# Optimization experiments

Hardware: AMD Instinct MI355X
Metric: run time of the kernel (lower is better)

The kernel has to match this reference:

```python
import jax, jax.numpy as jnp
import numpy as np

N_NODES = 32768
N_GRAPHS = 16
N_PER = N_NODES // N_GRAPHS  # 2048 nodes per graph
N_EDGES = 262144
D = 128      # node_state_dim
DE = 64      # edge_state_dim
H = 256      # edge hidden / message dim (= 2*D, required by matching prop)
NH = 256     # node MLP hidden


def _mlp2(x, W1, b1, W2, b2):
    # Linear -> ReLU -> Linear (torch nn.Linear convention: y = x @ W.T + b)
    return jax.nn.relu(x @ W1.T + b1) @ W2.T + b2


def setup_inputs() -> dict:
    key = jax.random.key(0)
    ks = jax.random.split(key, 16)
    s = 0.1  # edge_net_init_scale-ish small init
    inp = {
        "node_states": jax.random.normal(ks[0], (N_NODES, D), jnp.float32),
        "edge_features": jax.random.normal(ks[1], (N_EDGES, DE), jnp.float32),
        "from_idx": jax.random.randint(ks[2], (N_EDGES,), 0, N_NODES, jnp.int32),
        "to_idx": jax.random.randint(ks[3], (N_EDGES,), 0, N_NODES, jnp.int32),
        "graph_idx": jnp.repeat(jnp.arange(N_GRAPHS, dtype=jnp.int32), N_PER),
        "n_graphs": N_GRAPHS,
        # forward message net: Linear(2D+DE -> H), Linear(H -> H)
        "Wm1": jax.random.normal(ks[4], (H, 2 * D + DE), jnp.float32) * s,
        "bm1": jnp.zeros((H,), jnp.float32),
        "Wm2": jax.random.normal(ks[5], (H, H), jnp.float32) * s,
        "bm2": jnp.zeros((H,), jnp.float32),
        # reverse message net (separate params)
        "Wr1": jax.random.normal(ks[6], (H, 2 * D + DE), jnp.float32) * s,
        "br1": jnp.zeros((H,), jnp.float32),
        "Wr2": jax.random.normal(ks[7], (H, H), jnp.float32) * s,
        "br2": jnp.zeros((H,), jnp.float32),
        # node update MLP: Linear(4D -> NH), Linear(NH -> D)
        "Wn1": jax.random.normal(ks[8], (NH, 4 * D), jnp.float32) * s,
        "bn1": jnp.zeros((NH,), jnp.float32),
        "Wn2": jax.random.normal(ks[9], (D, NH), jnp.float32) * s,
        "bn2": jnp.zeros((D,), jnp.float32),
    }
    return inp


def _forward(node_states, edge_features, from_idx, to_idx, n_graphs,
             Wm1, bm1, Wm2, bm2, Wr1, br1, Wr2, br2, Wn1, bn1, Wn2, bn2):
    n = node_states.shape[0]
    fs = node_states[from_idx]   # [E, D] gather
    ts = node_states[to_idx]     # [E, D]
    # forward direction: messages -> scatter-add into to_idx
    m_fwd = _mlp2(jnp.concatenate([fs, ts, edge_features], -1), Wm1, bm1, Wm2, bm2)
    agg = jax.ops.segment_sum(m_fwd, to_idx, num_segments=n)
    # reverse direction: swap endpoints, scatter-add into from_idx
    m_rev = _mlp2(jnp.concatenate([ts, fs, edge_features], -1), Wr1, br1, Wr2, br2)
    agg = agg + jax.ops.segment_sum(m_rev, from_idx, num_segments=n)

    # cross-graph dual-softmax attention over (i, i+1) graph pairs.
    # graph_idx is contiguous equal-size blocks -> reshape partitioning.
    n_per = n // n_graphs
    d = node_states.reshape(n_graphs // 2, 2, n_per, -1)
    x, y = d[:, 0], d[:, 1]                      # [P, Np, D] each
    a = jnp.einsum('pid,pjd->pij', x, y)         # dotproduct similarity
    a_x = jax.nn.softmax(a, axis=2)              # softmax over y per x-row
    a_y = jax.nn.softmax(a, axis=1)              # softmax over x per y-col
    attn_x = jnp.einsum('pij,pjd->pid', a_x, y)  # [P, Np, D]
    attn_y = jnp.einsum('pij,pid->pjd', a_y, x)  # [P, Np, D]
    cross = jnp.stack([attn_x, attn_y], axis=1).reshape(n, -1)

    attention_input = node_states - cross
    node_inputs = jnp.concatenate([agg, attention_input, node_states], -1)  # [N, 4D]
    mlp_out = _mlp2(node_inputs, Wn1, bn1, Wn2, bn2)
    return node_states + mlp_out  # residual update


def reference(node_states, edge_features, from_idx, to_idx, graph_idx, n_graphs,
              Wm1, bm1, Wm2, bm2, Wr1, br1, Wr2, br2, Wn1, bn1, Wn2, bn2):
    return _forward(node_states, edge_features, from_idx, to_idx, int(n_graphs),
                    Wm1, bm1, Wm2, bm2, Wr1, br1, Wr2, br2, Wn1, bn1, Wn2, bn2)
```

## Files before the change

kernel.cpp:

```cpp
#include <hip/hip_runtime.h>


typedef __bf16 bf16_t;
typedef __bf16 bf16x8 __attribute__((ext_vector_type(8)));
typedef __bf16 bf16x4 __attribute__((ext_vector_type(4)));
typedef float  f32x4  __attribute__((ext_vector_type(4)));

#define MFMA16(a,b,c) __builtin_amdgcn_mfma_f32_16x16x32_bf16((a),(b),(c),0,0,0)

constexpr int NNODES = 32768;
constexpr int NEDGES = 262144;
constexpr int DD = 128;
constexpr int HH = 256;

__device__ __forceinline__ bf16x8 cvt8(f32x4 a, f32x4 b){
  bf16x8 r;
  r[0]=(bf16_t)a[0]; r[1]=(bf16_t)a[1]; r[2]=(bf16_t)a[2]; r[3]=(bf16_t)a[3];
  r[4]=(bf16_t)b[0]; r[5]=(bf16_t)b[1]; r[6]=(bf16_t)b[2]; r[7]=(bf16_t)b[3];
  return r;
}

__global__ void cvt_kernel(const float* __restrict__ in, bf16_t* __restrict__ out, int n){
  int i = (blockIdx.x*256 + threadIdx.x)*4;
  if (i < n){
    f32x4 v = *(const f32x4*)(in + i);
    bf16x4 o; o[0]=(bf16_t)v[0]; o[1]=(bf16_t)v[1]; o[2]=(bf16_t)v[2]; o[3]=(bf16_t)v[3];
    *(bf16x4*)(out + i) = o;
  }
}

__global__ void cvt_wp_kernel(const float* __restrict__ Wm1, const float* __restrict__ Wr1,
                              bf16_t* __restrict__ wp){
  int idx = (blockIdx.x*256 + threadIdx.x)*4;
  int n = idx >> 7, k = idx & 127;
  const float* W = (n < 512) ? Wm1 : Wr1;
  int row = n & 255;
  int colbase = ((n >> 8) & 1) * 128;
  f32x4 v = *(const f32x4*)(W + (size_t)row*320 + colbase + k);
  bf16x4 o; o[0]=(bf16_t)v[0]; o[1]=(bf16_t)v[1]; o[2]=(bf16_t)v[2]; o[3]=(bf16_t)v[3];
  *(bf16x4*)(wp + idx) = o;
}

__global__ void pack_wc_kernel(const float* __restrict__ Wm1, const float* __restrict__ Wr1,
                               bf16_t* __restrict__ wc){
  int g = blockIdx.x*256 + threadIdx.x;
  int part = g >> 11, gg = g & 2047;
  int tile = gg >> 6, lane = gg & 63;
  int kc = tile >> 4, nt = tile & 15;
  int lr = lane & 15, lk = lane >> 4;
  const float* W = part ? Wr1 : Wm1;
  int row = nt*16 + lr;
  int col = 256 + kc*32 + lk*8;
  f32x4 v0 = *(const f32x4*)(W + (size_t)row*320 + col);
  f32x4 v1 = *(const f32x4*)(W + (size_t)row*320 + col + 4);
  *(bf16x8*)(wc + (size_t)g*8) = cvt8(v0,v1);
}

__global__ void pack_wn2_kernel(const float* __restrict__ Wn2, bf16_t* __restrict__ out){
  int g = blockIdx.x*256 + threadIdx.x;
  int tile = g >> 6, lane = g & 63;
  int kc = tile >> 3, nt = tile & 7;
  int lr = lane & 15, lk = lane >> 4;
  int row = nt*16 + lr;
  int col = kc*32 + lk*8;
  f32x4 v0 = *(const f32x4*)(Wn2 + (size_t)row*256 + col);
  f32x4 v1 = *(const f32x4*)(Wn2 + (size_t)row*256 + col + 4);
  *(bf16x8*)(out + (size_t)g*8) = cvt8(v0,v1);
}

__global__ void hist_kernel(const int* __restrict__ to_idx, const int* __restrict__ from_idx,
                            int* __restrict__ cnt_to, int* __restrict__ cnt_from){
  int e = blockIdx.x*256 + threadIdx.x;
  if (e < NEDGES){
    atomicAdd(&cnt_to[to_idx[e]], 1);
    atomicAdd(&cnt_from[from_idx[e]], 1);
  }
}

__global__ void scan_kernel(int* __restrict__ cnt, int* __restrict__ start){
  __shared__ int sums[1024];
  const int t = threadIdx.x;
  int local[32]; int s = 0;
  #pragma unroll
  for (int j=0;j<32;j++){ local[j] = cnt[t*32+j]; s += local[j]; }
  sums[t] = s; __syncthreads();
  #pragma unroll
  for (int d=1; d<1024; d<<=1){
    int v = (t>=d) ? sums[t-d] : 0;
    __syncthreads();
    sums[t] += v;
    __syncthreads();
  }
  int off = sums[t] - s;
  #pragma unroll
  for (int j=0;j<32;j++){
    start[t*32+j] = off;
    cnt[t*32+j]   = off;
    off += local[j];
  }
  if (t == 1023) start[32768] = sums[1023];
}

__global__ void place_kernel(const int* __restrict__ to_idx, const int* __restrict__ from_idx,
                             int* __restrict__ cur_to, int* __restrict__ cur_from,
                             int* __restrict__ eid_to, int* __restrict__ eid_from,
                             int* __restrict__ rowv_to, int* __restrict__ rowv_from){
  int e = blockIdx.x*256 + threadIdx.x;
  if (e < NEDGES){
    int vt = to_idx[e];
    int p = atomicAdd(&cur_to[vt], 1);
    eid_to[p] = e;
    rowv_to[p] = vt;
    int vf = from_idx[e];
    int q = atomicAdd(&cur_from[vf], 1);
    eid_from[q] = e;
    rowv_from[q] = vf;
  }
}

__global__ __launch_bounds__(256,3) void proj_kernel(
    const float* __restrict__ ns, const bf16_t* __restrict__ Wp,
    bf16_t* __restrict__ P1, bf16_t* __restrict__ P2)
{
  constexpr int XS = 136;
  constexpr int CS = 264;
  __shared__ bf16_t Xs[64*XS];
  __shared__ bf16_t Cs[64*CS];
  const int tid = threadIdx.x;
  const int rb = blockIdx.x*64;
  const int cb = blockIdx.y;
  #pragma unroll
  for (int it=0; it<8; ++it){
    int c = tid + it*256;
    int row = c >> 5, co = (c & 31)*4;
    f32x4 v = *(const f32x4*)(ns + (size_t)(rb+row)*DD + co);
    bf16x4 o; o[0]=(bf16_t)v[0]; o[1]=(bf16_t)v[1]; o[2]=(bf16_t)v[2]; o[3]=(bf16_t)v[3];
    *(bf16x4*)&Xs[row*XS + co] = o;
  }
  __syncthreads();
  const int lane = tid & 63, wave = tid >> 6, lr = lane & 15, lk = lane >> 4;
  const bf16_t* Wb = Wp + (size_t)cb*256*128;
  f32x4 acc[16];
  #pragma unroll
  for (int nt=0;nt<16;nt++) acc[nt] = (f32x4){0.f,0.f,0.f,0.f};
  #pragma unroll
  for (int kc=0;kc<4;kc++){
    bf16x8 a = *(const bf16x8*)&Xs[(wave*16 + lr)*XS + kc*32 + lk*8];
    #pragma unroll
    for (int nt=0;nt<16;nt++){
      bf16x8 b = *(const bf16x8*)&Wb[(size_t)(nt*16 + lr)*128 + kc*32 + lk*8];
      acc[nt] = MFMA16(a,b,acc[nt]);
    }
  }
  #pragma unroll
  for (int nt=0;nt<16;nt++)
    #pragma unroll
    for (int r=0;r<4;r++)
      Cs[(wave*16 + lk*4 + r)*CS + nt*16 + lr] = (bf16_t)acc[nt][r];
  __syncthreads();
  bf16_t* P = cb ? P2 : P1;
  #pragma unroll
  for (int it=0; it<8; ++it){
    int c = tid + it*256;
    int row = c >> 5, co = (c & 31)*8;
    *(bf16x8*)&P[(size_t)(rb+row)*HH + co] = *(const bf16x8*)&Cs[row*CS + co];
  }
}

__global__ __launch_bounds__(256,4) void edge_agg_kernel(
    const float* __restrict__ ef, const bf16_t* __restrict__ Wc,
    const int* __restrict__ eid, const int* __restrict__ oth,
    const int* __restrict__ rowv, const int* __restrict__ start,
    const bf16_t* __restrict__ P1, const bf16_t* __restrict__ P2,
    const float* __restrict__ b1,
    float* __restrict__ partial, bf16_t* __restrict__ aggh)
{
  constexpr int CS = 264;
  __shared__ bf16_t Cs[64*CS];
  __shared__ int es[64], os[64], vs[64];
  const int tid = threadIdx.x;
  const int rb = blockIdx.x*64;
  if (tid < 64){
    int e = eid[rb + tid];
    es[tid] = e;
    os[tid] = oth[e];
    vs[tid] = rowv[rb + tid];
  }
  __syncthreads();

  const int lane = tid & 63, wave = tid >> 6, lr = lane & 15, lk = lane >> 4;
  {
    const float* arow = ef + (size_t)es[wave*16 + lr]*64;
    bf16x8 a0, a1;
    {
      f32x4 v0 = *(const f32x4*)(arow + lk*8);
      f32x4 v1 = *(const f32x4*)(arow + lk*8 + 4);
      a0 = cvt8(v0,v1);
      f32x4 w0 = *(const f32x4*)(arow + 32 + lk*8);
      f32x4 w1 = *(const f32x4*)(arow + 32 + lk*8 + 4);
      a1 = cvt8(w0,w1);
    }
    #pragma unroll
    for (int p=0;p<2;p++){
      f32x4 acc[8];
      #pragma unroll
      for (int nt=0;nt<8;nt++) acc[nt] = (f32x4){0.f,0.f,0.f,0.f};
      #pragma unroll
      for (int nt=0;nt<8;nt++){
        bf16x8 b0 = *(const bf16x8*)&Wc[(size_t)((0*16 + p*8 + nt)*64 + lane)*8];
        acc[nt] = MFMA16(a0,b0,acc[nt]);
        bf16x8 b1v = *(const bf16x8*)&Wc[(size_t)((1*16 + p*8 + nt)*64 + lane)*8];
        acc[nt] = MFMA16(a1,b1v,acc[nt]);
      }
      #pragma unroll
      for (int nt=0;nt<8;nt++)
        #pragma unroll
        for (int r=0;r<4;r++)
          Cs[(wave*16 + lk*4 + r)*CS + (p*8+nt)*16 + lr] = (bf16_t)acc[nt][r];
    }
  }
  __syncthreads();

  const int c8 = (tid & 31) * 8;
  const int rbase = (tid >> 5) * 8;
  {
    f32x4 b1a = *(const f32x4*)(b1 + c8);
    f32x4 b1b = *(const f32x4*)(b1 + c8 + 4);
    #pragma unroll
    for (int j=0;j<8;j++){
      const int row = rbase + j;
      bf16x8 cs = *(const bf16x8*)&Cs[row*CS + c8];
      bf16x8 p1 = *(const bf16x8*)&P1[(size_t)os[row]*HH + c8];
      bf16x8 p2 = *(const bf16x8*)&P2[(size_t)vs[row]*HH + c8];
      bf16x8 o;
      #pragma unroll
      for (int k=0;k<4;k++){
        o[k]   = (bf16_t)fmaxf((float)cs[k]   + (float)p1[k]   + (float)p2[k]   + b1a[k], 0.f);
        o[4+k] = (bf16_t)fmaxf((float)cs[4+k] + (float)p1[4+k] + (float)p2[4+k] + b1b[k], 0.f);
      }
      *(bf16x8*)&Cs[row*CS + c8] = o;
    }
  }
  __syncthreads();

  const int c = tid;
  float runsum = 0.f;
  int curv = vs[0];
  for (int row=0; row<64; ++row){
    const int v = vs[row];
    if (v != curv){
      const int s0 = start[curv], s1 = start[curv+1];
      if (s0 >= rb && s1 <= rb+64)
        aggh[(size_t)curv*HH + c] = (bf16_t)runsum;
      else
        partial[((size_t)curv*2 + (s0 >= rb ? 0 : 1))*HH + c] = runsum;
      runsum = 0.f; curv = v;
    }
    runsum += (float)Cs[row*CS + c];
  }
  {
    const int s0 = start[curv], s1 = start[curv+1];
    if (s0 >= rb && s1 <= rb+64)
      aggh[(size_t)curv*HH + c] = (bf16_t)runsum;
    else
      partial[((size_t)curv*2 + (s0 >= rb ? 0 : 1))*HH + c] = runsum;
  }
}

__global__ __launch_bounds__(256) void combine_kernel(
    const float* __restrict__ partial, const int* __restrict__ start,
    bf16_t* __restrict__ aggh)
{
  const int tid = threadIdx.x;
  const int v = blockIdx.x*8 + (tid>>5);
  const int c0 = (tid & 31)*8;
  const int s0 = start[v], s1 = start[v+1];
  if (s1 == s0){
    bf16x8 z;
    #pragma unroll
    for (int j=0;j<8;j++) z[j] = (bf16_t)0.f;
    *(bf16x8*)&aggh[(size_t)v*HH + c0] = z;
  } else if ((s0>>6) != ((s1-1)>>6)){
    const float* p0 = partial + ((size_t)v*2    )*HH + c0;
    const float* p1 = partial + ((size_t)v*2 + 1)*HH + c0;
    f32x4 a0 = *(const f32x4*)p0;
    f32x4 a1 = *(const f32x4*)(p0+4);
    f32x4 c1 = *(const f32x4*)p1;
    f32x4 c2 = *(const f32x4*)(p1+4);
    bf16x8 o;
    #pragma unroll
    for (int j=0;j<4;j++){ o[j]=(bf16_t)(a0[j]+c1[j]); o[4+j]=(bf16_t)(a1[j]+c2[j]); }
    *(bf16x8*)&aggh[(size_t)v*HH + c0] = o;
  }
}

__global__ __launch_bounds__(256) void w2t_kernel(const float* __restrict__ Wm2, const float* __restrict__ Wr2,
                                                  bf16_t* __restrict__ wm2T, bf16_t* __restrict__ wr2T){
  __shared__ bf16_t t[64][72];
  const int bi = (blockIdx.x & 3)*64;
  const int bj = ((blockIdx.x>>2) & 3)*64;
  const int m  = blockIdx.x >> 4;
  const float* W = m ? Wr2 : Wm2;
  bf16_t* WT = m ? wr2T : wm2T;
  const int tid = threadIdx.x;
  #pragma unroll
  for (int it=0; it<16; ++it){
    int c = tid + it*256;
    int r = c >> 6, co = c & 63;
    t[r][co] = (bf16_t)W[(size_t)(bi+r)*256 + bj + co];
  }
  __syncthreads();
  #pragma unroll
  for (int it=0; it<16; ++it){
    int c = tid + it*256;
    int r = c >> 6, co = c & 63;
    WT[(size_t)(bj+r)*256 + bi + co] = t[co][r];
  }
}

__global__ __launch_bounds__(256,2) void wcat_gemm_kernel(
    const float* __restrict__ Wn1, const bf16_t* __restrict__ wm2T, const bf16_t* __restrict__ wr2T,
    bf16_t* __restrict__ wcat)
{
  constexpr int XS = 264, CS = 264;
  __shared__ bf16_t Xs[64*XS];
  __shared__ bf16_t Cs[64*CS];
  const int tid = threadIdx.x;
  const int rb = blockIdx.x*64;
  const int cb = blockIdx.y;
  const bf16_t* BT = cb ? wr2T : wm2T;
  #pragma unroll
  for (int it=0; it<16; ++it){
    int c = tid + it*256;
    int row = c >> 6, co = (c & 63)*4;
    f32x4 v = *(const f32x4*)(Wn1 + (size_t)(rb+row)*512 + co);
    bf16x4 o; o[0]=(bf16_t)v[0]; o[1]=(bf16_t)v[1]; o[2]=(bf16_t)v[2]; o[3]=(bf16_t)v[3];
    *(bf16x4*)&Xs[row*XS + co] = o;
  }
  __syncthreads();
  const int lane = tid & 63, wave = tid >> 6, lr = lane & 15, lk = lane >> 4;
  f32x4 acc[16];
  #pragma unroll
  for (int nt=0;nt<16;nt++) acc[nt] = (f32x4){0.f,0.f,0.f,0.f};
  #pragma unroll
  for (int kc=0;kc<8;kc++){
    bf16x8 a = *(const bf16x8*)&Xs[(wave*16 + lr)*XS + kc*32 + lk*8];
    #pragma unroll
    for (int nt=0;nt<16;nt++){
      bf16x8 b = *(const bf16x8*)&BT[(size_t)(nt*16 + lr)*256 + kc*32 + lk*8];
      acc[nt] = MFMA16(a,b,acc[nt]);
    }
  }
  #pragma unroll
  for (int nt=0;nt<16;nt++)
    #pragma unroll
    for (int r=0;r<4;r++)
      Cs[(wave*16 + lk*4 + r)*CS + nt*16 + lr] = (bf16_t)acc[nt][r];
  __syncthreads();
  const int nt_base = rb >> 4;
  #pragma unroll
  for (int it=0; it<8; ++it){
    int g = tid + it*256;
    int tile = g >> 6, lane2 = g & 63;
    int kc_l = tile >> 2, nt_l = tile & 3;
    int lr2 = lane2 & 15, lk2 = lane2 >> 4;
    bf16x8 v = *(const bf16x8*)&Cs[(nt_l*16 + lr2)*CS + kc_l*32 + lk2*8];
    *(bf16x8*)&wcat[(size_t)(((cb*8 + kc_l)*16 + nt_base + nt_l)*64 + lane2)*8] = v;
  }
}

__global__ void wcat_copy_kernel(const float* __restrict__ Wn1, bf16_t* __restrict__ wcat){
  int g = blockIdx.x*256 + threadIdx.x;
  int tile = g >> 6, lane = g & 63;
  int kc = tile >> 4, nt = tile & 15;
  int lr = lane & 15, lk = lane >> 4;
  int row = nt*16 + lr;
  int col = 256 + kc*32 + lk*8;
  f32x4 v0 = *(const f32x4*)(Wn1 + (size_t)row*512 + col);
  f32x4 v1 = *(const f32x4*)(Wn1 + (size_t)row*512 + col + 4);
  *(bf16x8*)&wcat[(size_t)(((16 + kc)*16 + nt)*64 + lane)*8] = cvt8(v0,v1);
}

__global__ __launch_bounds__(256) void uw_kernel(const float* __restrict__ Wn1,
    const float* __restrict__ bm2, const float* __restrict__ br2,
    float* __restrict__ u, float* __restrict__ w){
  const int n = threadIdx.x;
  float su=0.f, sw=0.f;
  for (int j=0;j<256;j+=4){
    f32x4 wv = *(const f32x4*)(Wn1 + (size_t)n*512 + j);
    f32x4 bu = *(const f32x4*)(bm2 + j);
    f32x4 bw = *(const f32x4*)(br2 + j);
    #pragma unroll
    for (int q=0;q<4;q++){ su += wv[q]*bu[q]; sw += wv[q]*bw[q]; }
  }
  u[n]=su; w[n]=sw;
}

__global__ __launch_bounds__(256) void nst_kernel(const float* __restrict__ ns, bf16_t* __restrict__ nsT){
  constexpr int XS2 = 136;
  __shared__ bf16_t Xs[64*XS2];
  const int tid = threadIdx.x;
  const int nb = blockIdx.x*64;
  #pragma unroll
  for (int it=0; it<8; ++it){
    int c = tid + it*256;
    int rowl = c >> 5, co = (c & 31)*4;
    f32x4 v = *(const f32x4*)(ns + (size_t)(nb+rowl)*DD + co);
    bf16x4 o; o[0]=(bf16_t)v[0]; o[1]=(bf16_t)v[1]; o[2]=(bf16_t)v[2]; o[3]=(bf16_t)v[3];
    *(bf16x4*)&Xs[rowl*XS2 + co] = o;
  }
  __syncthreads();
  const int sb = nb >> 11;
  const int jb = nb & 2047;
  bf16_t* outp = nsT + (size_t)sb*DD*2048 + jb;
  #pragma unroll
  for (int it=0; it<4; ++it){
    int c = tid + it*256;
    int d = c >> 3, g8 = (c & 7)*8;
    bf16x8 o;
    #pragma unroll
    for (int k=0;k<8;k++){
      int s64 = g8 + k;
      int t32 = s64 >> 5, s = s64 & 31;
      int m = (s & 1) ? (16 + (s>>1)) : (s>>1);
      o[k] = Xs[(t32*32 + m)*XS2 + d];
    }
    *(bf16x8*)(outp + (size_t)d*2048 + g8) = o;
  }
}

__global__ __launch_bounds__(256,2) void attn_kernel(
    const bf16_t* __restrict__ nsB, const bf16_t* __restrict__ nsT,
    const float* __restrict__ ns, bf16_t* __restrict__ attnB)
{
  constexpr int KS = 136;
  constexpr int VS = 40;
  constexpr int PS = 40;
  __shared__ bf16_t Ks[2][32*KS];
  __shared__ bf16_t Vt[2][128*VS];
  __shared__ bf16_t Ps[64*PS];
  const int tid = threadIdx.x;
  const int lane = tid & 63, wave = tid >> 6, lr = lane & 15, lk = lane >> 4;
  const int bx = blockIdx.x;
  const int qt = bx & 31, side = (bx>>5)&1, p = bx>>6;
  const size_t qbase = (size_t)p*4096 + (size_t)side*2048 + (size_t)qt*64;
  const int sbkv = p*2 + (side^1);
  const bf16_t* Kv = nsB + ((size_t)p*4096 + (size_t)(side^1)*2048)*DD;
  const bf16_t* Vp = nsT + (size_t)sbkv*DD*2048;

  bf16x8 qf[4];
  {
    const bf16_t* qrow = nsB + (qbase + wave*16 + lr)*DD;
    #pragma unroll
    for (int kc=0;kc<4;kc++) qf[kc] = *(const bf16x8*)(qrow + kc*32 + lk*8);
  }
  float ls[4] = {0.f,0.f,0.f,0.f};
  f32x4 acco[8];
  #pragma unroll
  for (int nt=0;nt<8;nt++) acco[nt]=(f32x4){0.f,0.f,0.f,0.f};

  const int krow0 = tid>>4,        kcol = (tid&15)*8;
  const int vd0   = tid>>2,        vsl  = (tid&3)*8;
  bf16x8 kreg0, kreg1, vreg0, vreg1;

  auto load_tile = [&](int t){
    const bf16_t* kp = Kv + (size_t)t*32*DD;
    kreg0 = *(const bf16x8*)(kp + (size_t)krow0*DD + kcol);
    kreg1 = *(const bf16x8*)(kp + (size_t)(krow0+16)*DD + kcol);
    const bf16_t* vp = Vp + t*32;
    vreg0 = *(const bf16x8*)(vp + (size_t)vd0*2048 + vsl);
    vreg1 = *(const bf16x8*)(vp + (size_t)(vd0+64)*2048 + vsl);
  };
  auto store_tile = [&](int b){
    *(bf16x8*)&Ks[b][krow0*KS + kcol]      = kreg0;
    *(bf16x8*)&Ks[b][(krow0+16)*KS + kcol] = kreg1;
    *(bf16x8*)&Vt[b][vd0*VS + vsl]         = vreg0;
    *(bf16x8*)&Vt[b][(vd0+64)*VS + vsl]    = vreg1;
  };

  load_tile(0);
  store_tile(0);
  load_tile(1);
  __syncthreads();
  int cur = 0;
  for (int t=0; t<64; ++t){
    if (t+1 < 64){
      store_tile(cur^1);
      if (t+2 < 64) load_tile(t+2);
    }
    f32x4 s0 = (f32x4){0.f,0.f,0.f,0.f}, s1 = (f32x4){0.f,0.f,0.f,0.f};
    #pragma unroll
    for (int kc=0;kc<4;kc++){
      bf16x8 b0 = *(const bf16x8*)&Ks[cur][lr*KS      + kc*32 + lk*8];
      bf16x8 b1 = *(const bf16x8*)&Ks[cur][(16+lr)*KS + kc*32 + lk*8];
      s0 = MFMA16(qf[kc], b0, s0);
      s1 = MFMA16(qf[kc], b1, s1);
    }
    #pragma unroll
    for (int r=0;r<4;r++){
      float p0 = __expf(s0[r] - 40.f);
      float p1 = __expf(s1[r] - 40.f);
      ls[r] += p0 + p1;
      union { bf16_t h[2]; unsigned u; } pk;
      pk.h[0] = (bf16_t)p0; pk.h[1] = (bf16_t)p1;
      *(unsigned*)&Ps[(wave*16 + lk*4 + r)*PS + 2*lr] = pk.u;
    }
    asm volatile("s_waitcnt lgkmcnt(0)" ::: "memory");
    __builtin_amdgcn_sched_barrier(0);
    bf16x8 pa = *(const bf16x8*)&Ps[(wave*16 + lr)*PS + lk*8];
    #pragma unroll
    for (int nt=0;nt<8;nt++){
      bf16x8 vb = *(const bf16x8*)&Vt[cur][(nt*16+lr)*VS + lk*8];
      acco[nt] = MFMA16(pa, vb, acco[nt]);
    }
    __syncthreads();
    cur ^= 1;
  }
  #pragma unroll
  for (int r=0;r<4;r++){
    float v = ls[r];
    v += __shfl_xor(v,1); v += __shfl_xor(v,2);
    v += __shfl_xor(v,4); v += __shfl_xor(v,8);
    ls[r] = 1.f/v;
  }
  #pragma unroll
  for (int nt=0;nt<8;nt++){
    const int col = nt*16 + lr;
    #pragma unroll
    for (int r=0;r<4;r++){
      const size_t row = qbase + wave*16 + lk*4 + r;
      attnB[row*DD + col] = (bf16_t)(ns[row*DD + col] - acco[nt][r]*ls[r]);
    }
  }
}

__global__ __launch_bounds__(256,2) void node_mlp_kernel(
    const bf16_t* __restrict__ agghf, const bf16_t* __restrict__ agghr,
    const bf16_t* __restrict__ attnB, const bf16_t* __restrict__ nsB,
    const float* __restrict__ ns,
    const bf16_t* __restrict__ wcat, const float* __restrict__ bn1,
    const float* __restrict__ uvec, const float* __restrict__ wvec,
    const int* __restrict__ start_to, const int* __restrict__ start_from,
    const bf16_t* __restrict__ Wn2b, const float* __restrict__ bn2,
    float* __restrict__ out)
{
  __shared__ __align__(16) bf16_t As[32*768];
  bf16_t* Hs = As;
  const int tid = threadIdx.x;
  const int lane = tid & 63, wave = tid >> 6, lr = lane & 15, lk = lane >> 4;
  const int rb = blockIdx.x*32;

  bf16x8 stg[12];
  int dsta[12];
  #pragma unroll
  for (int it=0; it<12; ++it){
    const int db = it*4096 + tid*16;
    const int row = db / 1536;
    const int within = db - row*1536;
    const size_t node = (size_t)(rb + row);
    const char* s0 = (const char*)agghf + (node<<9) + within;
    const char* s1 = (const char*)agghr + (node<<9) + (within-512);
    const char* s2 = (const char*)attnB + (node<<8) + (within-1024);
    const char* s3 = (const char*)nsB   + (node<<8) + (within-1280);
    const char* src = within < 512 ? s0 : (within < 1024 ? s1 : (within < 1280 ? s2 : s3));
    stg[it] = *(const bf16x8*)src;
    dsta[it] = row*1536 + (within ^ ((row & 7) << 4));
  }
  #pragma unroll
  for (int it=0; it<12; ++it)
    *(bf16x8*)((char*)As + dsta[it]) = stg[it];
  __syncthreads();

  const int cg = wave >> 1;
  const int colbase = cg * 128;
  const int arow = (wave & 1)*16 + lr;
  const unsigned abase = (unsigned)arow * 1536u;
  const unsigned asw = ((unsigned)(arow & 7)) << 4;
  f32x4 acc[8];
  #pragma unroll
  for (int nt=0;nt<8;nt++) acc[nt] = (f32x4){0.f,0.f,0.f,0.f};
  #pragma unroll
  for (int kc=0; kc<24; ++kc){
    const unsigned y = (unsigned)(kc*64 + lk*16);
    bf16x8 a = *(const bf16x8*)((const char*)As + abase + (y ^ asw));
    #pragma unroll
    for (int nt=0;nt<8;nt++){
      bf16x8 b = *(const bf16x8*)&wcat[(size_t)((kc*16 + cg*8 + nt)*64 + lane)*8];
      acc[nt] = MFMA16(a,b,acc[nt]);
    }
  }
  __syncthreads();

  const int r0 = rb + (wave&1)*16 + lk*4;
  float dt[4], df[4];
  #pragma unroll
  for (int r=0;r<4;r++){
    dt[r] = (float)(start_to[r0+r+1]   - start_to[r0+r]);
    df[r] = (float)(start_from[r0+r+1] - start_from[r0+r]);
  }
  #pragma unroll
  for (int nt=0;nt<8;nt++){
    const int col = colbase + nt*16 + lr;
    const float bias = bn1[col];
    const float uu = uvec[col], ww = wvec[col];
    #pragma unroll
    for (int r=0;r<4;r++){
      float v = acc[nt][r] + bias + dt[r]*uu + df[r]*ww;
      v = v > 0.f ? v : 0.f;
      Hs[((wave&1)*16 + lk*4 + r)*264 + col] = (bf16_t)v;
    }
  }
  __syncthreads();

  const int cb2 = cg * 64;
  f32x4 acc2[4];
  #pragma unroll
  for (int nt=0;nt<4;nt++) acc2[nt] = (f32x4){0.f,0.f,0.f,0.f};
  #pragma unroll
  for (int kc=0;kc<8;kc++){
    bf16x8 a = *(const bf16x8*)&Hs[((wave&1)*16 + lr)*264 + kc*32 + lk*8];
    #pragma unroll
    for (int nt=0;nt<4;nt++){
      bf16x8 b = *(const bf16x8*)&Wn2b[(size_t)((kc*8 + cg*4 + nt)*64 + lane)*8];
      acc2[nt] = MFMA16(a,b,acc2[nt]);
    }
  }
  #pragma unroll
  for (int nt=0;nt<4;nt++){
    const int col = cb2 + nt*16 + lr;
    const float bias = bn2[col];
    #pragma unroll
    for (int r=0;r<4;r++){
      const size_t rr = (size_t)(r0 + r);
      out[rr*DD + col] = acc2[nt][r] + bias + ns[rr*DD + col];
    }
  }
}

extern "C" void kernel_launch(void* const* d_in, const int* in_sizes, int n_in,
                              void* d_out, int out_size, void* d_ws, size_t ws_size,
                              hipStream_t stream) {
  const float* ns  = (const float*)d_in[0];
  const float* ef  = (const float*)d_in[1];
  const int* from_idx = (const int*)d_in[2];
  const int* to_idx   = (const int*)d_in[3];
  const float* Wm1 = (const float*)d_in[6];  const float* bm1 = (const float*)d_in[7];
  const float* Wm2 = (const float*)d_in[8];  const float* bm2 = (const float*)d_in[9];
  const float* Wr1 = (const float*)d_in[10]; const float* br1 = (const float*)d_in[11];
  const float* Wr2 = (const float*)d_in[12]; const float* br2 = (const float*)d_in[13];
  const float* Wn1 = (const float*)d_in[14]; const float* bn1 = (const float*)d_in[15];
  const float* Wn2 = (const float*)d_in[16]; const float* bn2 = (const float*)d_in[17];

  char* ws = (char*)d_ws;
  float*  partial  = (float*)(ws);
  int*    rowv_to   = (int*)(ws + 67108864);
  int*    rowv_from = (int*)(ws + 68157440);
  bf16_t* P1t    = (bf16_t*)(ws + 134217728);
  bf16_t* P2t    = (bf16_t*)(ws + 150994944);
  bf16_t* aggh_f = (bf16_t*)(ws + 167772160);
  bf16_t* aggh_r = (bf16_t*)(ws + 184549376);
  bf16_t* wpb  = (bf16_t*)(ws + 201326592);
  bf16_t* wcb  = (bf16_t*)(ws + 201588736);
  bf16_t* wn2b = (bf16_t*)(ws + 201654272);
  int* cur_to     = (int*)(ws + 202244096);
  int* cur_from   = (int*)(ws + 202375168);
  int* start_to   = (int*)(ws + 202506240);
  int* start_from = (int*)(ws + 202637320);
  int* eid_to     = (int*)(ws + 202768400);
  int* eid_from   = (int*)(ws + 203816976);
  bf16_t* attnB = (bf16_t*)(ws);
  bf16_t* nsB   = (bf16_t*)(ws + 33554432);
  bf16_t* nsT   = (bf16_t*)(ws + 41943040);
  bf16_t* wm2T  = (bf16_t*)(ws + 50331648);
  bf16_t* wr2T  = (bf16_t*)(ws + 50462720);
  bf16_t* wcat  = (bf16_t*)(ws + 50593792);
  float*  uvec  = (float*) (ws + 50987008);
  float*  wvec  = (float*) (ws + 50988032);

  hipMemsetAsync(cur_to, 0, 2*NNODES*sizeof(int), stream);

  cvt_wp_kernel<<<128, 256, 0, stream>>>(Wm1, Wr1, wpb);
  pack_wc_kernel<<<16, 256, 0, stream>>>(Wm1, Wr1, wcb);
  pack_wn2_kernel<<<16, 256, 0, stream>>>(Wn2, wn2b);

  hist_kernel<<<NEDGES/256, 256, 0, stream>>>(to_idx, from_idx, cur_to, cur_from);
  scan_kernel<<<1, 1024, 0, stream>>>(cur_to, start_to);
  scan_kernel<<<1, 1024, 0, stream>>>(cur_from, start_from);
  place_kernel<<<NEDGES/256, 256, 0, stream>>>(to_idx, from_idx, cur_to, cur_from,
      eid_to, eid_from, rowv_to, rowv_from);

  proj_kernel<<<dim3(NNODES/64, 2), 256, 0, stream>>>(ns, wpb, P1t, P2t);
  edge_agg_kernel<<<NEDGES/64, 256, 0, stream>>>(ef, wcb, eid_to, from_idx,
      rowv_to, start_to, P1t, P2t, bm1, partial, aggh_f);
  combine_kernel<<<NNODES/8, 256, 0, stream>>>(partial, start_to, aggh_f);

  proj_kernel<<<dim3(NNODES/64, 2), 256, 0, stream>>>(ns, wpb + 512*128, P1t, P2t);
  edge_agg_kernel<<<NEDGES/64, 256, 0, stream>>>(ef, wcb + 256*64, eid_from, to_idx,
      rowv_from, start_from, P1t, P2t, br1, partial, aggh_r);
  combine_kernel<<<NNODES/8, 256, 0, stream>>>(partial, start_from, aggh_r);

  cvt_kernel<<<4096, 256, 0, stream>>>(ns, nsB, NNODES*DD);
  nst_kernel<<<NNODES/64, 256, 0, stream>>>(ns, nsT);
  w2t_kernel<<<32, 256, 0, stream>>>(Wm2, Wr2, wm2T, wr2T);
  wcat_gemm_kernel<<<dim3(4,2), 256, 0, stream>>>(Wn1, wm2T, wr2T, wcat);
  wcat_copy_kernel<<<32, 256, 0, stream>>>(Wn1, wcat);
  uw_kernel<<<1, 256, 0, stream>>>(Wn1, bm2, br2, uvec, wvec);

  attn_kernel<<<512, 256, 0, stream>>>(nsB, nsT, ns, attnB);

  node_mlp_kernel<<<NNODES/32, 256, 0, stream>>>(aggh_f, aggh_r, attnB, nsB, ns,
      wcat, bn1, uvec, wvec, start_to, start_from, wn2b, bn2, (float*)d_out);
}
```

Measured before the change: 456.5 us.

## Split attention over KV halves with combine kernel; fuse bf16 cast into transpose

The attention kernel now splits the 2048 keys into two halves, launching 1024 blocks instead of 512 so more of the GPU stays occupied. Each block writes unnormalized fp32 partial outputs and row sums, and a new combine kernel adds them, normalizes, and subtracts from node states. The standalone fp32-to-bf16 conversion kernel is folded into the transpose kernel, which removes one launch and one read of node states. The split adds extra fp32 partial traffic (about 32 MB written and read back), and launch bounds are raised to 3 blocks per CU.

```diff
diff --git a/kernel.cpp b/kernel.cpp
--- a/kernel.cpp
+++ b/kernel.cpp
@@ -18,15 +18,6 @@
   r[0]=(bf16_t)a[0]; r[1]=(bf16_t)a[1]; r[2]=(bf16_t)a[2]; r[3]=(bf16_t)a[3];
   r[4]=(bf16_t)b[0]; r[5]=(bf16_t)b[1]; r[6]=(bf16_t)b[2]; r[7]=(bf16_t)b[3];
   return r;
-}
-
-__global__ void cvt_kernel(const float* __restrict__ in, bf16_t* __restrict__ out, int n){
-  int i = (blockIdx.x*256 + threadIdx.x)*4;
-  if (i < n){
-    f32x4 v = *(const f32x4*)(in + i);
-    bf16x4 o; o[0]=(bf16_t)v[0]; o[1]=(bf16_t)v[1]; o[2]=(bf16_t)v[2]; o[3]=(bf16_t)v[3];
-    *(bf16x4*)(out + i) = o;
-  }
 }
 
 __global__ void cvt_wp_kernel(const float* __restrict__ Wm1, const float* __restrict__ Wr1,
@@ -396,7 +387,9 @@
   u[n]=su; w[n]=sw;
 }
 
-__global__ __launch_bounds__(256) void nst_kernel(const float* __restrict__ ns, bf16_t* __restrict__ nsT){
+__global__ __launch_bounds__(256) void nst_kernel(const float* __restrict__ ns,
+                                                  bf16_t* __restrict__ nsT,
+                                                  bf16_t* __restrict__ nsB){
   constexpr int XS2 = 136;
   __shared__ bf16_t Xs[64*XS2];
   const int tid = threadIdx.x;
@@ -408,6 +401,7 @@
     f32x4 v = *(const f32x4*)(ns + (size_t)(nb+rowl)*DD + co);
     bf16x4 o; o[0]=(bf16_t)v[0]; o[1]=(bf16_t)v[1]; o[2]=(bf16_t)v[2]; o[3]=(bf16_t)v[3];
     *(bf16x4*)&Xs[rowl*XS2 + co] = o;
+    *(bf16x4*)&nsB[(size_t)(nb+rowl)*DD + co] = o;
   }
   __syncthreads();
   const int sb = nb >> 11;
@@ -429,9 +423,9 @@
   }
 }
 
-__global__ __launch_bounds__(256,2) void attn_kernel(
+__global__ __launch_bounds__(256,3) void attn_kernel(
     const bf16_t* __restrict__ nsB, const bf16_t* __restrict__ nsT,
-    const float* __restrict__ ns, bf16_t* __restrict__ attnB)
+    float* __restrict__ Opart, float* __restrict__ lpart)
 {
   constexpr int KS = 136;
   constexpr int VS = 40;
@@ -442,11 +436,11 @@
   const int tid = threadIdx.x;
   const int lane = tid & 63, wave = tid >> 6, lr = lane & 15, lk = lane >> 4;
   const int bx = blockIdx.x;
-  const int qt = bx & 31, side = (bx>>5)&1, p = bx>>6;
+  const int qt = bx & 31, side = (bx>>5)&1, p = (bx>>6)&7, kvh = bx>>9;
   const size_t qbase = (size_t)p*4096 + (size_t)side*2048 + (size_t)qt*64;
   const int sbkv = p*2 + (side^1);
-  const bf16_t* Kv = nsB + ((size_t)p*4096 + (size_t)(side^1)*2048)*DD;
-  const bf16_t* Vp = nsT + (size_t)sbkv*DD*2048;
+  const bf16_t* Kv = nsB + ((size_t)p*4096 + (size_t)(side^1)*2048)*DD + (size_t)kvh*32*32*DD;
+  const bf16_t* Vp = nsT + (size_t)sbkv*DD*2048 + (size_t)kvh*32*32;
 
   bf16x8 qf[4];
   {
@@ -483,10 +477,10 @@
   load_tile(1);
   __syncthreads();
   int cur = 0;
-  for (int t=0; t<64; ++t){
-    if (t+1 < 64){
+  for (int t=0; t<32; ++t){
+    if (t+1 < 32){
       store_tile(cur^1);
-      if (t+2 < 64) load_tile(t+2);
+      if (t+2 < 32) load_tile(t+2);
     }
     f32x4 s0 = (f32x4){0.f,0.f,0.f,0.f}, s1 = (f32x4){0.f,0.f,0.f,0.f};
     #pragma unroll
@@ -521,17 +515,40 @@
     float v = ls[r];
     v += __shfl_xor(v,1); v += __shfl_xor(v,2);
     v += __shfl_xor(v,4); v += __shfl_xor(v,8);
-    ls[r] = 1.f/v;
-  }
-  #pragma unroll
-  for (int nt=0;nt<8;nt++){
-    const int col = nt*16 + lr;
-    #pragma unroll
-    for (int r=0;r<4;r++){
-      const size_t row = qbase + wave*16 + lk*4 + r;
-      attnB[row*DD + col] = (bf16_t)(ns[row*DD + col] - acco[nt][r]*ls[r]);
-    }
-  }
+    ls[r] = v;
+  }
+  float* Op = Opart + (size_t)kvh*NNODES*DD;
+  #pragma unroll
+  for (int r=0;r<4;r++){
+    const size_t row = qbase + wave*16 + lk*4 + r;
+    if (lr == 0) lpart[(size_t)kvh*NNODES + row] = ls[r];
+    #pragma unroll
+    for (int nt=0;nt<8;nt++)
+      Op[row*DD + nt*16 + lr] = acco[nt][r];
+  }
+}
+
+__global__ __launch_bounds__(256) void attn_combine_kernel(
+    const float* __restrict__ ns, const float* __restrict__ Opart,
+    const float* __restrict__ lpart, bf16_t* __restrict__ attnB)
+{
+  const int tid = threadIdx.x;
+  const int row = blockIdx.x*16 + (tid >> 4);
+  const int c0 = (tid & 15)*8;
+  const float inv = 1.f/(lpart[row] + lpart[NNODES + row]);
+  const float* o0 = Opart + (size_t)row*DD + c0;
+  const float* o1 = Opart + (size_t)NNODES*DD + (size_t)row*DD + c0;
+  const float* nr = ns + (size_t)row*DD + c0;
+  f32x4 a0 = *(const f32x4*)o0,      a1 = *(const f32x4*)(o0+4);
+  f32x4 b0 = *(const f32x4*)o1,      b1 = *(const f32x4*)(o1+4);
+  f32x4 n0 = *(const f32x4*)nr,      n1 = *(const f32x4*)(nr+4);
+  bf16x8 o;
+  #pragma unroll
+  for (int j=0;j<4;j++){
+    o[j]   = (bf16_t)(n0[j] - (a0[j]+b0[j])*inv);
+    o[4+j] = (bf16_t)(n1[j] - (a1[j]+b1[j])*inv);
+  }
+  *(bf16x8*)&attnB[(size_t)row*DD + c0] = o;
 }
 
 __global__ __launch_bounds__(256,2) void node_mlp_kernel(
@@ -676,6 +693,8 @@
   bf16_t* wcat  = (bf16_t*)(ws + 50593792);
   float*  uvec  = (float*) (ws + 50987008);
   float*  wvec  = (float*) (ws + 50988032);
+  float*  Opart = (float*) (ws + 69206016);
+  float*  lpart = (float*) (ws + 102760448);
 
   hipMemsetAsync(cur_to, 0, 2*NNODES*sizeof(int), stream);
 
@@ -699,14 +718,14 @@
       rowv_from, start_from, P1t, P2t, br1, partial, aggh_r);
   combine_kernel<<<NNODES/8, 256, 0, stream>>>(partial, start_from, aggh_r);
 
-  cvt_kernel<<<4096, 256, 0, stream>>>(ns, nsB, NNODES*DD);
-  nst_kernel<<<NNODES/64, 256, 0, stream>>>(ns, nsT);
+  nst_kernel<<<NNODES/64, 256, 0, stream>>>(ns, nsT, nsB);
   w2t_kernel<<<32, 256, 0, stream>>>(Wm2, Wr2, wm2T, wr2T);
   wcat_gemm_kernel<<<dim3(4,2), 256, 0, stream>>>(Wn1, wm2T, wr2T, wcat);
   wcat_copy_kernel<<<32, 256, 0, stream>>>(Wn1, wcat);
   uw_kernel<<<1, 256, 0, stream>>>(Wn1, bm2, br2, uvec, wvec);
 
-  attn_kernel<<<512, 256, 0, stream>>>(nsB, nsT, ns, attnB);
+  attn_kernel<<<1024, 256, 0, stream>>>(nsB, nsT, Opart, lpart);
+  attn_combine_kernel<<<NNODES/16, 256, 0, stream>>>(ns, Opart, lpart, attnB);
 
   node_mlp_kernel<<<NNODES/32, 256, 0, stream>>>(aggh_f, aggh_r, attnB, nsB, ns,
       wcat, bn1, uvec, wvec, start_to, start_from, wn2b, bn2, (float*)d_out);
```

New measurement: 452.8 us. No clear change (-0.8%).
